# Optimization experiments

Hardware: AMD Instinct MI355X
Metric: run time of the kernel (lower is better)

Reference implementation:

```python
import jax, jax.numpy as jnp
import numpy as np

HEAD_NUM = 16

def setup_inputs() -> dict:
    key = jax.random.key(0)
    k1, k2, k3, k4, k5 = jax.random.split(key, 5)
    B, S, F = 4, 2048, 1024
    return {
        "X": jax.random.normal(k1, (B, S, F), dtype=jnp.float32),
        "residual_score": jax.random.normal(k2, (B, S, F), dtype=jnp.float32),
        "wq": jax.random.normal(k3, (F, F), dtype=jnp.float32) * 0.05,
        "wk": jax.random.normal(k4, (F, F), dtype=jnp.float32) * 0.05,
        "wv": jax.random.normal(k5, (F, F), dtype=jnp.float32) * 0.05,
    }

def reference(X, residual_score, wq, wk, wv):
    B, S, F = X.shape
    H = HEAD_NUM
    D = F // H  # head dim
    # Original scales logits by sqrt(seq_len / head_num), not sqrt(head_dim).
    scale = jnp.sqrt(jnp.asarray(S / H, dtype=X.dtype))
    # QKV projections: [B,S,F] @ [F,F] -> [B,S,F], then split features into heads -> [B,H,S,D]
    def proj(w):
        y = jnp.einsum('bsf,fg->bsg', X, w)
        return y.reshape(B, S, H, D).transpose(0, 2, 1, 3)
    q, k, v = proj(wq), proj(wk), proj(wv)
    logits = jnp.einsum('bhsd,bhtd->bhst', q, k) / scale  # [B,H,S,S]
    attn = jax.nn.softmax(logits, axis=-1)
    effect = jnp.einsum('bhst,bhtd->bhsd', attn, v)  # [B,H,S,D]
    all_effects = effect.transpose(0, 2, 1, 3).reshape(B, S, F)
    out = all_effects + residual_score
    return (out, out)
```

## Files before the change

kernel.cpp:

```cpp
#include <hip/hip_runtime.h>
#include <hip/hip_bf16.h>
#include <stdint.h>

#define B_ 4
#define S_ 2048
#define F_ 1024
#define H_ 16
#define D_ 64
#define M_ (B_*S_)
#define OUTHALF ((size_t)B_*S_*F_)
#define KVB 64
#define QBLK 256

typedef __attribute__((ext_vector_type(4))) float f32x4;
typedef __attribute__((ext_vector_type(8))) short bf16x8;

__device__ __forceinline__ short f2bf(float f) {
  __hip_bfloat16 h = __float2bfloat16(f);
  return *reinterpret_cast<short*>(&h);
}

__device__ __forceinline__ void gl2lds16(const short* g, short* l) {
  __builtin_amdgcn_global_load_lds(
      (const __attribute__((address_space(1))) uint32_t*)g,
      (__attribute__((address_space(3))) uint32_t*)l, 16, 0, 0);
}

#define VMCNT_BAR(N)                                            \
  do {                                                          \
    asm volatile("s_waitcnt vmcnt(" #N ")" ::: "memory");       \
    __builtin_amdgcn_s_barrier();                               \
    asm volatile("" ::: "memory");                              \
  } while (0)

__global__ __launch_bounds__(256) void convert_x(const float* __restrict__ X,
                                                 short* __restrict__ Xb) {
  int i = (blockIdx.x * 256 + threadIdx.x) * 8;
  f32x4 a = *(const f32x4*)(X + i);
  f32x4 b = *(const f32x4*)(X + i + 4);
  bf16x8 o;
  o[0]=f2bf(a[0]); o[1]=f2bf(a[1]); o[2]=f2bf(a[2]); o[3]=f2bf(a[3]);
  o[4]=f2bf(b[0]); o[5]=f2bf(b[1]); o[6]=f2bf(b[2]); o[7]=f2bf(b[3]);
  *(bf16x8*)(Xb + i) = o;
}

__global__ __launch_bounds__(256) void transpose_w(
    const float* __restrict__ wq, const float* __restrict__ wk, const float* __restrict__ wv,
    short* __restrict__ tq, short* __restrict__ tk, short* __restrict__ tv) {
  const float* W = blockIdx.z == 0 ? wq : (blockIdx.z == 1 ? wk : wv);
  short* T = blockIdx.z == 0 ? tq : (blockIdx.z == 1 ? tk : tv);
  __shared__ float tile[32][33];
  int tx = threadIdx.x, ty = threadIdx.y;
  int x = blockIdx.x * 32 + tx;
  int y0 = blockIdx.y * 32;
  #pragma unroll
  for (int j = ty; j < 32; j += 8) tile[j][tx] = W[(size_t)(y0 + j) * F_ + x];
  __syncthreads();
  int x2 = y0 + tx;
  int y2 = blockIdx.x * 32;
  #pragma unroll
  for (int j = ty; j < 32; j += 8) T[(size_t)(y2 + j) * F_ + x2] = f2bf(tile[tx][j]);
}

__global__ __launch_bounds__(256) void gemm_qkv(
    const short* __restrict__ Xb,
    const short* __restrict__ Wtq, const short* __restrict__ Wtk, const short* __restrict__ Wtv,
    short* __restrict__ Qb, short* __restrict__ Kb, short* __restrict__ Vt) {
  __shared__ short As[2][128 * 32];
  __shared__ short Bs[2][128 * 32];
  const int z = blockIdx.z;
  const short* Wt = z == 0 ? Wtq : (z == 1 ? Wtk : Wtv);
  const int m0 = blockIdx.x * 128, n0 = blockIdx.y * 128;
  const int tid = threadIdx.x, wid = tid >> 6, lane = tid & 63;
  const int wm = wid >> 1, wn = wid & 1;
  const int l15 = lane & 15, l4 = lane >> 4;

  f32x4 acc[4][4];
  #pragma unroll
  for (int i = 0; i < 4; ++i)
    #pragma unroll
    for (int j = 0; j < 4; ++j) acc[i][j] = {0.f, 0.f, 0.f, 0.f};

  const int srow = wid * 32 + (lane >> 2);
  const int scol = (lane & 3) * 8;

  auto stage = [&](int buf, int k0) {
    gl2lds16(Xb + (size_t)(m0 + srow) * F_ + k0 + scol,      &As[buf][(wid * 32) * 32]);
    gl2lds16(Xb + (size_t)(m0 + srow + 16) * F_ + k0 + scol, &As[buf][(wid * 32 + 16) * 32]);
    gl2lds16(Wt + (size_t)(n0 + srow) * F_ + k0 + scol,      &Bs[buf][(wid * 32) * 32]);
    gl2lds16(Wt + (size_t)(n0 + srow + 16) * F_ + k0 + scol, &Bs[buf][(wid * 32 + 16) * 32]);
  };

  stage(0, 0);
  const int NT = F_ / 32;
  for (int t = 0; t < NT; ++t) {
    const int buf = t & 1;
    if (t + 1 < NT) {
      stage(buf ^ 1, (t + 1) * 32);
      VMCNT_BAR(4);
    } else {
      VMCNT_BAR(0);
    }
    bf16x8 a[4], b[4];
    #pragma unroll
    for (int mf = 0; mf < 4; ++mf)
      a[mf] = *(const bf16x8*)&As[buf][(wm * 64 + mf * 16 + l15) * 32 + l4 * 8];
    #pragma unroll
    for (int nf = 0; nf < 4; ++nf)
      b[nf] = *(const bf16x8*)&Bs[buf][(wn * 64 + nf * 16 + l15) * 32 + l4 * 8];
    __builtin_amdgcn_s_setprio(1);
    #pragma unroll
    for (int mf = 0; mf < 4; ++mf)
      #pragma unroll
      for (int nf = 0; nf < 4; ++nf)
        acc[mf][nf] = __builtin_amdgcn_mfma_f32_16x16x32_bf16(a[mf], b[nf], acc[mf][nf], 0, 0, 0);
    __builtin_amdgcn_s_setprio(0);
    __builtin_amdgcn_s_barrier();
    asm volatile("" ::: "memory");
  }

  const float qscale = 0.12751784477559752f;
  #pragma unroll
  for (int mf = 0; mf < 4; ++mf)
    #pragma unroll
    for (int nf = 0; nf < 4; ++nf)
      #pragma unroll
      for (int r = 0; r < 4; ++r) {
        float v = acc[mf][nf][r];
        int row = m0 + wm * 64 + mf * 16 + l4 * 4 + r;
        int col = n0 + wn * 64 + nf * 16 + l15;
        int bb = row >> 11, s = row & 2047, h = col >> 6, d = col & 63;
        if (z == 0)
          Qb[((size_t)(bb * H_ + h) * S_ + s) * D_ + d] = f2bf(v * qscale);
        else if (z == 1)
          Kb[((size_t)(bb * H_ + h) * S_ + s) * D_ + d] = f2bf(v);
        else {
          int s5 = s & 31;
          int sp = (s & ~31) | (((s5 >> 2) & 3) << 3) | (((s5 >> 4) & 1) << 2) | (s5 & 3);
          Vt[((size_t)(bb * H_ + h) * D_ + d) * S_ + sp] = f2bf(v);
        }
      }
}

__global__ __launch_bounds__(512, 4) void attn_kernel(
    const short* __restrict__ Qb, const short* __restrict__ Kb, const short* __restrict__ Vt,
    const float* __restrict__ resid, float* __restrict__ out) {
  __shared__ short Ks[2][KVB][64];
  __shared__ short Vs[2][D_][KVB];
  const int bh = blockIdx.x;
  const int b = bh >> 4, h = bh & 15;
  const int qbase = blockIdx.y * QBLK;
  const int wid = threadIdx.x >> 6, lane = threadIdx.x & 63;
  const int l15 = lane & 15, l4 = lane >> 4;
  const short* Qp = Qb + (size_t)bh * S_ * D_;
  const short* Kp = Kb + (size_t)bh * S_ * D_;
  const short* Vp = Vt + (size_t)bh * D_ * S_;

  bf16x8 bq[2][2];
  #pragma unroll
  for (int g = 0; g < 2; ++g) {
    int qr = qbase + wid * 32 + g * 16 + l15;
    bq[g][0] = *(const bf16x8*)&Qp[qr * D_ + l4 * 8];
    bq[g][1] = *(const bf16x8*)&Qp[qr * D_ + 32 + l4 * 8];
  }

  bf16x8 aOnes;
  {
    short onebf = (short)0x3F80;
    #pragma unroll
    for (int i = 0; i < 8; ++i) aOnes[i] = (l15 == 0) ? onebf : (short)0;
  }

  const int sr = wid * 8 + (lane >> 3);
  const int ssrc = ((lane & 7) ^ (lane >> 3)) * 8;

  f32x4 acc[2][4];
  f32x4 accl[2];
  #pragma unroll
  for (int g = 0; g < 2; ++g) {
    accl[g] = {0.f, 0.f, 0.f, 0.f};
    #pragma unroll
    for (int df = 0; df < 4; ++df) acc[g][df] = {0.f, 0.f, 0.f, 0.f};
  }

  gl2lds16(Kp + (0 + sr) * D_ + ssrc, &Ks[0][wid * 8][0]);
  gl2lds16(Vp + (size_t)sr * S_ + 0 + ssrc, &Vs[0][wid * 8][0]);

  const int NT = S_ / KVB;
  for (int t = 0; t < NT; ++t) {
    const int buf = t & 1;
    __syncthreads();
    if (t + 1 < NT) {
      const int kv1 = (t + 1) * KVB;
      gl2lds16(Kp + (kv1 + sr) * D_ + ssrc, &Ks[buf ^ 1][wid * 8][0]);
      gl2lds16(Vp + (size_t)sr * S_ + kv1 + ssrc, &Vs[buf ^ 1][wid * 8][0]);
    }

    f32x4 sf[2][4];
    #pragma unroll
    for (int g = 0; g < 2; ++g)
      #pragma unroll
      for (int nf = 0; nf < 4; ++nf) sf[g][nf] = {0.f, 0.f, 0.f, 0.f};
    __builtin_amdgcn_s_setprio(1);
    #pragma unroll
    for (int nf = 0; nf < 4; ++nf) {
      int row = nf * 16 + l15;
      int c0 = (l4 ^ (row & 7)) * 8;
      int c1 = ((4 + l4) ^ (row & 7)) * 8;
      bf16x8 ak0 = *(const bf16x8*)&Ks[buf][row][c0];
      bf16x8 ak1 = *(const bf16x8*)&Ks[buf][row][c1];
      #pragma unroll
      for (int g = 0; g < 2; ++g) {
        sf[g][nf] = __builtin_amdgcn_mfma_f32_16x16x32_bf16(ak0, bq[g][0], sf[g][nf], 0, 0, 0);
        sf[g][nf] = __builtin_amdgcn_mfma_f32_16x16x32_bf16(ak1, bq[g][1], sf[g][nf], 0, 0, 0);
      }
    }
    __builtin_amdgcn_s_setprio(0);

    bf16x8 pb[2][2];
    #pragma unroll
    for (int g = 0; g < 2; ++g)
      #pragma unroll
      for (int bb = 0; bb < 2; ++bb) {
        bf16x8 p;
        #pragma unroll
        for (int r = 0; r < 4; ++r) {
          p[r]     = f2bf(__builtin_amdgcn_exp2f(sf[g][2 * bb][r]));
          p[4 + r] = f2bf(__builtin_amdgcn_exp2f(sf[g][2 * bb + 1][r]));
        }
        pb[g][bb] = p;
      }

    __builtin_amdgcn_s_setprio(1);
    #pragma unroll
    for (int bb = 0; bb < 2; ++bb) {
      #pragma unroll
      for (int df = 0; df < 4; ++df) {
        int row = df * 16 + l15;
        bf16x8 av = *(const bf16x8*)&Vs[buf][row][((4 * bb + l4) ^ (row & 7)) * 8];
        acc[0][df] = __builtin_amdgcn_mfma_f32_16x16x32_bf16(av, pb[0][bb], acc[0][df], 0, 0, 0);
        acc[1][df] = __builtin_amdgcn_mfma_f32_16x16x32_bf16(av, pb[1][bb], acc[1][df], 0, 0, 0);
      }
      accl[0] = __builtin_amdgcn_mfma_f32_16x16x32_bf16(aOnes, pb[0][bb], accl[0], 0, 0, 0);
      accl[1] = __builtin_amdgcn_mfma_f32_16x16x32_bf16(aOnes, pb[1][bb], accl[1], 0, 0, 0);
    }
    __builtin_amdgcn_s_setprio(0);
  }

  #pragma unroll
  for (int g = 0; g < 2; ++g) {
    float lg = __shfl(accl[g][0], l15);
    float rl = 1.f / lg;
    int s = qbase + wid * 32 + g * 16 + l15;
    #pragma unroll
    for (int df = 0; df < 4; ++df) {
      size_t oi = ((size_t)b * S_ + s) * F_ + h * D_ + df * 16 + l4 * 4;
      f32x4 rv = *(const f32x4*)&resid[oi];
      f32x4 ov;
      #pragma unroll
      for (int r = 0; r < 4; ++r) ov[r] = acc[g][df][r] * rl + rv[r];
      *(f32x4*)&out[oi] = ov;
      *(f32x4*)&out[oi + OUTHALF] = ov;
    }
  }
}

extern "C" void kernel_launch(void* const* d_in, const int* in_sizes, int n_in,
                              void* d_out, int out_size, void* d_ws, size_t ws_size,
                              hipStream_t stream) {
  (void)in_sizes; (void)n_in; (void)out_size; (void)ws_size;
  const float* X     = (const float*)d_in[0];
  const float* resid = (const float*)d_in[1];
  const float* wq    = (const float*)d_in[2];
  const float* wk    = (const float*)d_in[3];
  const float* wv    = (const float*)d_in[4];
  float* out = (float*)d_out;
  char* ws = (char*)d_ws;
  short* Xb  = (short*)(ws);
  short* Wtq = (short*)(ws + (16u << 20));
  short* Wtk = (short*)(ws + (18u << 20));
  short* Wtv = (short*)(ws + (20u << 20));
  short* Qb  = (short*)(ws + (22u << 20));
  short* Kb  = (short*)(ws + (38u << 20));
  short* Vt  = (short*)(ws + (54u << 20));

  convert_x<<<dim3((M_ * F_) / (256 * 8)), 256, 0, stream>>>(X, Xb);
  transpose_w<<<dim3(32, 32, 3), dim3(32, 8), 0, stream>>>(wq, wk, wv, Wtq, Wtk, Wtv);
  gemm_qkv<<<dim3(M_ / 128, F_ / 128, 3), 256, 0, stream>>>(Xb, Wtq, Wtk, Wtv, Qb, Kb, Vt);
  attn_kernel<<<dim3(B_ * H_, S_ / QBLK), 512, 0, stream>>>(Qb, Kb, Vt, resid, out);
}
```

Before: 174.4 us.

## Halve attention query block to 4 waves and compute row sums in VALU

Shrinks each attention block from 8 waves covering 256 queries to 4 waves covering 128 queries, doubling the grid to 1024 blocks. Each thread now issues two K and two V LDS loads per tile, with the swizzle computed from the row. The softmax denominator is no longer produced by extra MFMAs against a ones vector; it is summed from the fp32 exp values with two cross-lane shuffles per tile. This removes a fifth of the PV-stage MFMAs and may balance work better across CUs, at the cost of more K/V global traffic per query and added VALU and shuffle work.

```diff
diff --git a/kernel.cpp b/kernel.cpp
--- a/kernel.cpp
+++ b/kernel.cpp
@@ -10,7 +10,7 @@
 #define M_ (B_*S_)
 #define OUTHALF ((size_t)B_*S_*F_)
 #define KVB 64
-#define QBLK 256
+#define QBLK 128
 
 typedef __attribute__((ext_vector_type(4))) float f32x4;
 typedef __attribute__((ext_vector_type(8))) short bf16x8;
@@ -142,7 +142,7 @@
       }
 }
 
-__global__ __launch_bounds__(512, 4) void attn_kernel(
+__global__ __launch_bounds__(256) void attn_kernel(
     const short* __restrict__ Qb, const short* __restrict__ Kb, const short* __restrict__ Vt,
     const float* __restrict__ resid, float* __restrict__ out) {
   __shared__ short Ks[2][KVB][64];
@@ -164,27 +164,22 @@
     bq[g][1] = *(const bf16x8*)&Qp[qr * D_ + 32 + l4 * 8];
   }
 
-  bf16x8 aOnes;
-  {
-    short onebf = (short)0x3F80;
-    #pragma unroll
-    for (int i = 0; i < 8; ++i) aOnes[i] = (l15 == 0) ? onebf : (short)0;
-  }
-
-  const int sr = wid * 8 + (lane >> 3);
-  const int ssrc = ((lane & 7) ^ (lane >> 3)) * 8;
+  const int sr0 = wid * 16 + (lane >> 3);
+  const int sr1 = sr0 + 8;
+  const int sc0 = ((lane & 7) ^ (sr0 & 7)) * 8;
+  const int sc1 = ((lane & 7) ^ (sr1 & 7)) * 8;
 
   f32x4 acc[2][4];
-  f32x4 accl[2];
-  #pragma unroll
-  for (int g = 0; g < 2; ++g) {
-    accl[g] = {0.f, 0.f, 0.f, 0.f};
+  float lsum[2] = {0.f, 0.f};
+  #pragma unroll
+  for (int g = 0; g < 2; ++g)
     #pragma unroll
     for (int df = 0; df < 4; ++df) acc[g][df] = {0.f, 0.f, 0.f, 0.f};
-  }
-
-  gl2lds16(Kp + (0 + sr) * D_ + ssrc, &Ks[0][wid * 8][0]);
-  gl2lds16(Vp + (size_t)sr * S_ + 0 + ssrc, &Vs[0][wid * 8][0]);
+
+  gl2lds16(Kp + (0 + sr0) * D_ + sc0, &Ks[0][wid * 16][0]);
+  gl2lds16(Kp + (0 + sr1) * D_ + sc1, &Ks[0][wid * 16 + 8][0]);
+  gl2lds16(Vp + (size_t)sr0 * S_ + 0 + sc0, &Vs[0][wid * 16][0]);
+  gl2lds16(Vp + (size_t)sr1 * S_ + 0 + sc1, &Vs[0][wid * 16 + 8][0]);
 
   const int NT = S_ / KVB;
   for (int t = 0; t < NT; ++t) {
@@ -192,8 +187,10 @@
     __syncthreads();
     if (t + 1 < NT) {
       const int kv1 = (t + 1) * KVB;
-      gl2lds16(Kp + (kv1 + sr) * D_ + ssrc, &Ks[buf ^ 1][wid * 8][0]);
-      gl2lds16(Vp + (size_t)sr * S_ + kv1 + ssrc, &Vs[buf ^ 1][wid * 8][0]);
+      gl2lds16(Kp + (kv1 + sr0) * D_ + sc0, &Ks[buf ^ 1][wid * 16][0]);
+      gl2lds16(Kp + (kv1 + sr1) * D_ + sc1, &Ks[buf ^ 1][wid * 16 + 8][0]);
+      gl2lds16(Vp + (size_t)sr0 * S_ + kv1 + sc0, &Vs[buf ^ 1][wid * 16][0]);
+      gl2lds16(Vp + (size_t)sr1 * S_ + kv1 + sc1, &Vs[buf ^ 1][wid * 16 + 8][0]);
     }
 
     f32x4 sf[2][4];
@@ -218,18 +215,32 @@
     __builtin_amdgcn_s_setprio(0);
 
     bf16x8 pb[2][2];
-    #pragma unroll
-    for (int g = 0; g < 2; ++g)
+    float ps[2];
+    #pragma unroll
+    for (int g = 0; g < 2; ++g) {
+      float s0 = 0.f;
       #pragma unroll
       for (int bb = 0; bb < 2; ++bb) {
         bf16x8 p;
         #pragma unroll
         for (int r = 0; r < 4; ++r) {
-          p[r]     = f2bf(__builtin_amdgcn_exp2f(sf[g][2 * bb][r]));
-          p[4 + r] = f2bf(__builtin_amdgcn_exp2f(sf[g][2 * bb + 1][r]));
+          float p0 = __builtin_amdgcn_exp2f(sf[g][2 * bb][r]);
+          float p1 = __builtin_amdgcn_exp2f(sf[g][2 * bb + 1][r]);
+          p[r]     = f2bf(p0);
+          p[4 + r] = f2bf(p1);
+          s0 += p0 + p1;
         }
         pb[g][bb] = p;
       }
+      ps[g] = s0;
+    }
+    #pragma unroll
+    for (int g = 0; g < 2; ++g) {
+      float s0 = ps[g];
+      s0 += __shfl_xor(s0, 16);
+      s0 += __shfl_xor(s0, 32);
+      lsum[g] += s0;
+    }
 
     __builtin_amdgcn_s_setprio(1);
     #pragma unroll
@@ -241,16 +252,13 @@
         acc[0][df] = __builtin_amdgcn_mfma_f32_16x16x32_bf16(av, pb[0][bb], acc[0][df], 0, 0, 0);
         acc[1][df] = __builtin_amdgcn_mfma_f32_16x16x32_bf16(av, pb[1][bb], acc[1][df], 0, 0, 0);
       }
-      accl[0] = __builtin_amdgcn_mfma_f32_16x16x32_bf16(aOnes, pb[0][bb], accl[0], 0, 0, 0);
-      accl[1] = __builtin_amdgcn_mfma_f32_16x16x32_bf16(aOnes, pb[1][bb], accl[1], 0, 0, 0);
     }
     __builtin_amdgcn_s_setprio(0);
   }
 
   #pragma unroll
   for (int g = 0; g < 2; ++g) {
-    float lg = __shfl(accl[g][0], l15);
-    float rl = 1.f / lg;
+    float rl = 1.f / lsum[g];
     int s = qbase + wid * 32 + g * 16 + l15;
     #pragma unroll
     for (int df = 0; df < 4; ++df) {
@@ -287,5 +295,5 @@
   convert_x<<<dim3((M_ * F_) / (256 * 8)), 256, 0, stream>>>(X, Xb);
   transpose_w<<<dim3(32, 32, 3), dim3(32, 8), 0, stream>>>(wq, wk, wv, Wtq, Wtk, Wtv);
   gemm_qkv<<<dim3(M_ / 128, F_ / 128, 3), 256, 0, stream>>>(Xb, Wtq, Wtk, Wtv, Qb, Kb, Vt);
-  attn_kernel<<<dim3(B_ * H_, S_ / QBLK), 512, 0, stream>>>(Qb, Kb, Vt, resid, out);
-}
+  attn_kernel<<<dim3(B_ * H_, S_ / QBLK), 256, 0, stream>>>(Qb, Kb, Vt, resid, out);
+}
```

Result: slower. 205.8 us (+18.0%).

## Double KV tile to 128 and interleave exp with QK MFMAs

Applied to the files above, without the earlier changes.

Doubles the KV block per iteration from 64 to 128, so each step loads two K rows and two V rows per lane and the V swizzle widens to 16 chunks. This halves the number of loop iterations and barriers. The QK^T loop now converts each pair of score fragments to bf16 probabilities as soon as they are ready, which keeps fewer fp32 score registers live and lets exp overlap with MFMAs. It costs more LDS per buffer and more register pressure for the wider probability tiles.

```diff
diff --git a/kernel.cpp b/kernel.cpp
--- a/kernel.cpp
+++ b/kernel.cpp
@@ -9,7 +9,7 @@
 #define D_ 64
 #define M_ (B_*S_)
 #define OUTHALF ((size_t)B_*S_*F_)
-#define KVB 64
+#define KVB 128
 #define QBLK 256
 
 typedef __attribute__((ext_vector_type(4))) float f32x4;
@@ -171,8 +171,14 @@
     for (int i = 0; i < 8; ++i) aOnes[i] = (l15 == 0) ? onebf : (short)0;
   }
 
-  const int sr = wid * 8 + (lane >> 3);
-  const int ssrc = ((lane & 7) ^ (lane >> 3)) * 8;
+  const int ksr0 = wid * 16 + (lane >> 3);
+  const int ksr1 = ksr0 + 8;
+  const int ksc0 = ((lane & 7) ^ (ksr0 & 7)) * 8;
+  const int ksc1 = ((lane & 7) ^ (ksr1 & 7)) * 8;
+  const int vr0 = wid * 8 + (lane >> 4);
+  const int vr1 = vr0 + 4;
+  const int vsc0 = ((lane & 15) ^ (vr0 & 15)) * 8;
+  const int vsc1 = ((lane & 15) ^ (vr1 & 15)) * 8;
 
   f32x4 acc[2][4];
   f32x4 accl[2];
@@ -183,8 +189,10 @@
     for (int df = 0; df < 4; ++df) acc[g][df] = {0.f, 0.f, 0.f, 0.f};
   }
 
-  gl2lds16(Kp + (0 + sr) * D_ + ssrc, &Ks[0][wid * 8][0]);
-  gl2lds16(Vp + (size_t)sr * S_ + 0 + ssrc, &Vs[0][wid * 8][0]);
+  gl2lds16(Kp + (0 + ksr0) * D_ + ksc0, &Ks[0][wid * 16][0]);
+  gl2lds16(Kp + (0 + ksr1) * D_ + ksc1, &Ks[0][wid * 16 + 8][0]);
+  gl2lds16(Vp + (size_t)vr0 * S_ + 0 + vsc0, &Vs[0][wid * 8][0]);
+  gl2lds16(Vp + (size_t)vr1 * S_ + 0 + vsc1, &Vs[0][wid * 8 + 4][0]);
 
   const int NT = S_ / KVB;
   for (int t = 0; t < NT; ++t) {
@@ -192,52 +200,52 @@
     __syncthreads();
     if (t + 1 < NT) {
       const int kv1 = (t + 1) * KVB;
-      gl2lds16(Kp + (kv1 + sr) * D_ + ssrc, &Ks[buf ^ 1][wid * 8][0]);
-      gl2lds16(Vp + (size_t)sr * S_ + kv1 + ssrc, &Vs[buf ^ 1][wid * 8][0]);
-    }
-
-    f32x4 sf[2][4];
-    #pragma unroll
-    for (int g = 0; g < 2; ++g)
-      #pragma unroll
-      for (int nf = 0; nf < 4; ++nf) sf[g][nf] = {0.f, 0.f, 0.f, 0.f};
+      gl2lds16(Kp + (kv1 + ksr0) * D_ + ksc0, &Ks[buf ^ 1][wid * 16][0]);
+      gl2lds16(Kp + (kv1 + ksr1) * D_ + ksc1, &Ks[buf ^ 1][wid * 16 + 8][0]);
+      gl2lds16(Vp + (size_t)vr0 * S_ + kv1 + vsc0, &Vs[buf ^ 1][wid * 8][0]);
+      gl2lds16(Vp + (size_t)vr1 * S_ + kv1 + vsc1, &Vs[buf ^ 1][wid * 8 + 4][0]);
+    }
+
+    bf16x8 pb[2][4];
+    f32x4 sfp[2];
     __builtin_amdgcn_s_setprio(1);
     #pragma unroll
-    for (int nf = 0; nf < 4; ++nf) {
+    for (int nf = 0; nf < 8; ++nf) {
       int row = nf * 16 + l15;
       int c0 = (l4 ^ (row & 7)) * 8;
       int c1 = ((4 + l4) ^ (row & 7)) * 8;
       bf16x8 ak0 = *(const bf16x8*)&Ks[buf][row][c0];
       bf16x8 ak1 = *(const bf16x8*)&Ks[buf][row][c1];
-      #pragma unroll
-      for (int g = 0; g < 2; ++g) {
-        sf[g][nf] = __builtin_amdgcn_mfma_f32_16x16x32_bf16(ak0, bq[g][0], sf[g][nf], 0, 0, 0);
-        sf[g][nf] = __builtin_amdgcn_mfma_f32_16x16x32_bf16(ak1, bq[g][1], sf[g][nf], 0, 0, 0);
-      }
-    }
-    __builtin_amdgcn_s_setprio(0);
-
-    bf16x8 pb[2][2];
-    #pragma unroll
-    for (int g = 0; g < 2; ++g)
-      #pragma unroll
-      for (int bb = 0; bb < 2; ++bb) {
-        bf16x8 p;
+      f32x4 s0 = {0.f, 0.f, 0.f, 0.f}, s1 = {0.f, 0.f, 0.f, 0.f};
+      s0 = __builtin_amdgcn_mfma_f32_16x16x32_bf16(ak0, bq[0][0], s0, 0, 0, 0);
+      s0 = __builtin_amdgcn_mfma_f32_16x16x32_bf16(ak1, bq[0][1], s0, 0, 0, 0);
+      s1 = __builtin_amdgcn_mfma_f32_16x16x32_bf16(ak0, bq[1][0], s1, 0, 0, 0);
+      s1 = __builtin_amdgcn_mfma_f32_16x16x32_bf16(ak1, bq[1][1], s1, 0, 0, 0);
+      if ((nf & 1) == 0) {
+        sfp[0] = s0; sfp[1] = s1;
+      } else {
+        const int bb = nf >> 1;
+        bf16x8 p0, p1;
         #pragma unroll
         for (int r = 0; r < 4; ++r) {
-          p[r]     = f2bf(__builtin_amdgcn_exp2f(sf[g][2 * bb][r]));
-          p[4 + r] = f2bf(__builtin_amdgcn_exp2f(sf[g][2 * bb + 1][r]));
+          p0[r]     = f2bf(__builtin_amdgcn_exp2f(sfp[0][r]));
+          p0[4 + r] = f2bf(__builtin_amdgcn_exp2f(s0[r]));
+          p1[r]     = f2bf(__builtin_amdgcn_exp2f(sfp[1][r]));
+          p1[4 + r] = f2bf(__builtin_amdgcn_exp2f(s1[r]));
         }
-        pb[g][bb] = p;
+        pb[0][bb] = p0;
+        pb[1][bb] = p1;
       }
+    }
+    __builtin_amdgcn_s_setprio(0);
 
     __builtin_amdgcn_s_setprio(1);
     #pragma unroll
-    for (int bb = 0; bb < 2; ++bb) {
+    for (int bb = 0; bb < 4; ++bb) {
       #pragma unroll
       for (int df = 0; df < 4; ++df) {
         int row = df * 16 + l15;
-        bf16x8 av = *(const bf16x8*)&Vs[buf][row][((4 * bb + l4) ^ (row & 7)) * 8];
+        bf16x8 av = *(const bf16x8*)&Vs[buf][row][((4 * bb + l4) ^ (row & 15)) * 8];
         acc[0][df] = __builtin_amdgcn_mfma_f32_16x16x32_bf16(av, pb[0][bb], acc[0][df], 0, 0, 0);
         acc[1][df] = __builtin_amdgcn_mfma_f32_16x16x32_bf16(av, pb[1][bb], acc[1][df], 0, 0, 0);
       }
```

New measurement: 253.4 us. +45.3%, slower.
